# Kernel tuning notes

Hardware: AMD Instinct MI355X
Metric: run time of the kernel (lower is better)

The kernel has to match this reference:

```python
import jax, jax.numpy as jnp
import numpy as np

D = 1024        # d_model
H = 4           # num_heads
DK = D          # key_dim   (expand_k = 1.0)
DV = 2 * D      # value_dim (expand_v = 2.0)
HK = DK // H    # per-head key dim
HV = DV // H    # per-head value dim
KCONV = 4       # short conv kernel size
EPS = 1e-5
CHUNK = 64      # scan chunk size (checkpointing granularity)


def causal_conv_silu(x, w):
    # x: [B,T,C], w: [C,K] depthwise causal conv followed by silu
    B, T, C = x.shape
    K = w.shape[1]
    xp = jnp.pad(x, ((0, 0), (K - 1, 0), (0, 0)))
    y = sum(xp[:, i:i + T, :] * w[:, i] for i in range(K))
    return jax.nn.silu(y)


def l2norm(x):
    return x * jax.lax.rsqrt(jnp.sum(x * x, -1, keepdims=True) + 1e-6)


def _step(S, inp):
    # gated delta rule, one time step. S: [B,H,HK,HV]
    q_t, k_t, v_t, g_t, b_t = inp  # [B,H,HK],[B,H,HK],[B,H,HV],[B,H],[B,H]
    S = S * jnp.exp(g_t)[..., None, None]
    v_eff = (v_t - jnp.einsum('bhk,bhkv->bhv', k_t, S)) * b_t[..., None]
    S = S + k_t[..., None] * v_eff[..., None, :]
    o_t = jnp.einsum('bhk,bhkv->bhv', q_t, S)
    return S, o_t


@jax.checkpoint
def _chunk(S, ch):
    return jax.lax.scan(_step, S, ch)


def _forward(x, ln_w, ln_b, Wq, Wk, Wv, conv_q, conv_k, conv_v, Wb, Wa,
             A_log, dt_bias, Wg, norm_w, Wo):
    B, T, _ = x.shape
    # pre-LayerNorm
    mu = jnp.mean(x, -1, keepdims=True)
    var = jnp.mean((x - mu) ** 2, -1, keepdims=True)
    normed = (x - mu) * jax.lax.rsqrt(var + EPS) * ln_w + ln_b
    # projections + short conv + silu
    q = causal_conv_silu(normed @ Wq, conv_q)
    k = causal_conv_silu(normed @ Wk, conv_k)
    v = causal_conv_silu(normed @ Wv, conv_v)
    beta = jax.nn.sigmoid(normed @ Wb)                                # [B,T,H]
    g = -jnp.exp(A_log) * jax.nn.softplus(normed @ Wa + dt_bias)      # [B,T,H]
    q = l2norm(q.reshape(B, T, H, HK)) * (HK ** -0.5)
    k = l2norm(k.reshape(B, T, H, HK))
    v = v.reshape(B, T, H, HV)
    # chunked sequential scan over time
    nc = T // CHUNK
    def to_chunks(a):
        return jnp.moveaxis(a, 1, 0).reshape((nc, CHUNK, B) + a.shape[2:])
    qc, kc, vc, gc, bc = map(to_chunks, (q, k, v, g, beta))
    S0 = jnp.zeros((B, H, HK, HV), x.dtype)
    _, o = jax.lax.scan(_chunk, S0, (qc, kc, vc, gc, bc))
    o = jnp.moveaxis(o.reshape(T, B, H, HV), 0, 1)                    # [B,T,H,HV]
    # RMSNorm-swish output gate
    g_out = (normed @ Wg).reshape(B, T, H, HV)
    o = o * jax.lax.rsqrt(jnp.mean(o * o, -1, keepdims=True) + EPS) * norm_w
    o = o * g_out * jax.nn.sigmoid(g_out)
    return x + o.reshape(B, T, DV) @ Wo


def setup_inputs() -> dict:
    key = jax.random.key(0)
    ks = jax.random.split(key, 16)
    B, T = 4, 2048
    p = lambda k, shape, s=0.02: jax.random.normal(k, shape, jnp.float32) * s
    return {
        'x': jax.random.normal(ks[0], (B, T, D), jnp.float32),
        'ln_w': jnp.ones((D,), jnp.float32),
        'ln_b': jnp.zeros((D,), jnp.float32),
        'Wq': p(ks[1], (D, DK)),
        'Wk': p(ks[2], (D, DK)),
        'Wv': p(ks[3], (D, DV)),
        'conv_q': p(ks[4], (DK, KCONV), 0.1),
        'conv_k': p(ks[5], (DK, KCONV), 0.1),
        'conv_v': p(ks[6], (DV, KCONV), 0.1),
        'Wb': p(ks[7], (D, H)),
        'Wa': p(ks[8], (D, H)),
        'A_log': jnp.log(jax.random.uniform(ks[9], (H,), jnp.float32, 1.0, 16.0)),
        'dt_bias': jnp.log(jnp.expm1(jax.random.uniform(ks[10], (H,), jnp.float32, 0.001, 0.1))),
        'Wg': p(ks[11], (D, DV)),
        'norm_w': jnp.ones((HV,), jnp.float32),
        'Wo': p(ks[12], (DV, D)),
    }


def reference(x, ln_w, ln_b, Wq, Wk, Wv, conv_q, conv_k, conv_v, Wb, Wa,
              A_log, dt_bias, Wg, norm_w, Wo):
    return _forward(x, ln_w, ln_b, Wq, Wk, Wv, conv_q, conv_k, conv_v,
                    Wb, Wa, A_log, dt_bias, Wg, norm_w, Wo)
```

## Files before the change

### kernel.cpp

```cpp
#include <hip/hip_runtime.h>
#include <math.h>

#define BB 4
#define TT 2048
#define RTOT 8192
#define DD 1024
#define HH 4
#define DKC 1024
#define DVC 2048
#define HKC 256
#define HVC 512
#define NC 32
#define TILE_CV 32

typedef unsigned short u16;
typedef unsigned int u32;
typedef short bf8v __attribute__((ext_vector_type(8)));
typedef float f32x4 __attribute__((ext_vector_type(4)));

__device__ __forceinline__ float bf2f(u16 u) {
    union { float f; u32 i; } c; c.i = ((u32)u) << 16; return c.f;
}
__device__ __forceinline__ u16 f2bf(float f) {
    union { float f; u32 i; } c; c.f = f;
    const u32 i = c.i;
    return (u16)((i + 0x7FFFu + ((i >> 16) & 1u)) >> 16);
}
__device__ __forceinline__ float sigmoidf_(float x) { return 1.0f / (1.0f + expf(-x)); }
__device__ __forceinline__ f32x4 mfma16(bf8v a, bf8v b, f32x4 c) {
    return __builtin_amdgcn_mfma_f32_16x16x32_bf16(a, b, c, 0, 0, 0);
}

__global__ __launch_bounds__(256) void ln_kernel(const float* __restrict__ x,
                                                 const float* __restrict__ w,
                                                 const float* __restrict__ b,
                                                 u16* __restrict__ out) {
    const int row = blockIdx.x;
    const int tid = threadIdx.x;
    const int lane = tid & 63, wave = tid >> 6;
    const float4 xv = *(const float4*)&x[(size_t)row * DD + tid * 4];
    float s = xv.x + xv.y + xv.z + xv.w;
    float sq = xv.x * xv.x + xv.y * xv.y + xv.z * xv.z + xv.w * xv.w;
    for (int m = 32; m >= 1; m >>= 1) {
        s += __shfl_xor(s, m, 64);
        sq += __shfl_xor(sq, m, 64);
    }
    __shared__ float s1[4], s2[4];
    if (lane == 0) { s1[wave] = s; s2[wave] = sq; }
    __syncthreads();
    const float tot = s1[0] + s1[1] + s1[2] + s1[3];
    const float totq = s2[0] + s2[1] + s2[2] + s2[3];
    const float mean = tot * (1.0f / DD);
    const float var = totq * (1.0f / DD) - mean * mean;
    const float rstd = rsqrtf(var + 1e-5f);
    const float4 wv = *(const float4*)&w[tid * 4];
    const float4 bv = *(const float4*)&b[tid * 4];
    ushort4 o;
    o.x = f2bf((xv.x - mean) * rstd * wv.x + bv.x);
    o.y = f2bf((xv.y - mean) * rstd * wv.y + bv.y);
    o.z = f2bf((xv.z - mean) * rstd * wv.z + bv.z);
    o.w = f2bf((xv.w - mean) * rstd * wv.w + bv.w);
    *(ushort4*)&out[(size_t)row * DD + tid * 4] = o;
}

__global__ __launch_bounds__(256) void wconv_kernel(const float* __restrict__ W,
                                                    u16* __restrict__ WT, int K, int N) {
    __shared__ float tile[32][33];
    const int k0 = blockIdx.x * 32, n0 = blockIdx.y * 32;
    const int t = threadIdx.x;
    const int r = t >> 3, c4 = (t & 7) * 4;
    const float4 v = *(const float4*)&W[(size_t)(k0 + r) * N + n0 + c4];
    tile[r][c4 + 0] = v.x; tile[r][c4 + 1] = v.y;
    tile[r][c4 + 2] = v.z; tile[r][c4 + 3] = v.w;
    __syncthreads();
    ushort4 o;
    o.x = f2bf(tile[c4 + 0][r]); o.y = f2bf(tile[c4 + 1][r]);
    o.z = f2bf(tile[c4 + 2][r]); o.w = f2bf(tile[c4 + 3][r]);
    *(ushort4*)&WT[(size_t)(n0 + r) * K + k0 + c4] = o;
}

template <int OUTMODE>
__global__ __launch_bounds__(256, 2) void gemm_mfma(const u16* __restrict__ A,
                                                    const u16* __restrict__ BT,
                                                    void* __restrict__ Cv,
                                                    int M, int N, int K,
                                                    const float* __restrict__ Res) {
    __shared__ u16 As[128][40];
    __shared__ u16 Bs[128][40];
    const int tid = threadIdx.x;
    const int wave = tid >> 6, lane = tid & 63;
    const int quad = lane >> 4, l15 = lane & 15;
    const int wr = wave >> 1, wc = wave & 1;
    const int bn = blockIdx.x, bm = blockIdx.y;
    const int srow = tid >> 1, sh = (tid & 1) * 16;
    const u16* Ap = A + (size_t)(bm * 128 + srow) * K + sh;
    const u16* Bp = BT + (size_t)(bn * 128 + srow) * K + sh;
    f32x4 acc[4][4];
#pragma unroll
    for (int i = 0; i < 4; ++i)
#pragma unroll
        for (int j = 0; j < 4; ++j) acc[i][j] = (f32x4){0.f, 0.f, 0.f, 0.f};

    for (int k0 = 0; k0 < K; k0 += 32) {
        const bf8v a0 = *(const bf8v*)(Ap + k0);
        const bf8v a1 = *(const bf8v*)(Ap + k0 + 8);
        const bf8v b0 = *(const bf8v*)(Bp + k0);
        const bf8v b1 = *(const bf8v*)(Bp + k0 + 8);
        __syncthreads();
        *(bf8v*)&As[srow][sh] = a0;
        *(bf8v*)&As[srow][sh + 8] = a1;
        *(bf8v*)&Bs[srow][sh] = b0;
        *(bf8v*)&Bs[srow][sh + 8] = b1;
        __syncthreads();
        bf8v af[4], bfr[4];
#pragma unroll
        for (int i = 0; i < 4; ++i) af[i] = *(const bf8v*)&As[wr * 64 + i * 16 + l15][quad * 8];
#pragma unroll
        for (int j = 0; j < 4; ++j) bfr[j] = *(const bf8v*)&Bs[wc * 64 + j * 16 + l15][quad * 8];
#pragma unroll
        for (int i = 0; i < 4; ++i)
#pragma unroll
            for (int j = 0; j < 4; ++j)
                acc[i][j] = mfma16(af[i], bfr[j], acc[i][j]);
    }
#pragma unroll
    for (int i = 0; i < 4; ++i) {
        const int row = bm * 128 + wr * 64 + i * 16 + quad * 4;
#pragma unroll
        for (int j = 0; j < 4; ++j) {
            const int col = bn * 128 + wc * 64 + j * 16 + l15;
            if (OUTMODE == 0) {
                u16* C = (u16*)Cv;
#pragma unroll
                for (int r = 0; r < 4; ++r)
                    C[(size_t)(row + r) * N + col] = f2bf(acc[i][j][r]);
            } else {
                float* C = (float*)Cv;
#pragma unroll
                for (int r = 0; r < 4; ++r)
                    C[(size_t)(row + r) * N + col] = acc[i][j][r] + Res[(size_t)(row + r) * N + col];
            }
        }
    }
}

__global__ __launch_bounds__(256) void smallproj_kernel(const float* __restrict__ x,
                                                        const float* __restrict__ lnw,
                                                        const float* __restrict__ lnb,
                                                        const float* __restrict__ Wb,
                                                        const float* __restrict__ Wa,
                                                        const float* __restrict__ A_log,
                                                        const float* __restrict__ dt_bias,
                                                        float* __restrict__ beta,
                                                        float* __restrict__ gdec) {
    const int row = blockIdx.x;
    const int tid = threadIdx.x;
    const int lane = tid & 63, wave = tid >> 6;
    const float4 xv = *(const float4*)&x[(size_t)row * DD + tid * 4];
    float s = xv.x + xv.y + xv.z + xv.w;
    float sq = xv.x * xv.x + xv.y * xv.y + xv.z * xv.z + xv.w * xv.w;
    for (int m = 32; m >= 1; m >>= 1) {
        s += __shfl_xor(s, m, 64);
        sq += __shfl_xor(sq, m, 64);
    }
    __shared__ float s1[4], s2[4];
    if (lane == 0) { s1[wave] = s; s2[wave] = sq; }
    __syncthreads();
    const float mean = (s1[0] + s1[1] + s1[2] + s1[3]) * (1.0f / DD);
    const float var = (s2[0] + s2[1] + s2[2] + s2[3]) * (1.0f / DD) - mean * mean;
    const float rstd = rsqrtf(var + 1e-5f);
    const float4 wv = *(const float4*)&lnw[tid * 4];
    const float4 bv = *(const float4*)&lnb[tid * 4];
    float nv[4];
    nv[0] = (xv.x - mean) * rstd * wv.x + bv.x;
    nv[1] = (xv.y - mean) * rstd * wv.y + bv.y;
    nv[2] = (xv.z - mean) * rstd * wv.z + bv.z;
    nv[3] = (xv.w - mean) * rstd * wv.w + bv.w;
    float acc[8] = {};
#pragma unroll
    for (int j = 0; j < 4; ++j) {
        const int kk = tid * 4 + j;
        const float4 wb = ((const float4*)Wb)[kk];
        const float4 wa = ((const float4*)Wa)[kk];
        acc[0] += nv[j] * wb.x; acc[1] += nv[j] * wb.y; acc[2] += nv[j] * wb.z; acc[3] += nv[j] * wb.w;
        acc[4] += nv[j] * wa.x; acc[5] += nv[j] * wa.y; acc[6] += nv[j] * wa.z; acc[7] += nv[j] * wa.w;
    }
#pragma unroll
    for (int i = 0; i < 8; ++i)
        for (int m = 32; m >= 1; m >>= 1) acc[i] += __shfl_xor(acc[i], m, 64);
    __shared__ float sred[4][8];
    if (lane == 0)
#pragma unroll
        for (int i = 0; i < 8; ++i) sred[wave][i] = acc[i];
    __syncthreads();
    if (tid < 8) {
        const float sv = sred[0][tid] + sred[1][tid] + sred[2][tid] + sred[3][tid];
        if (tid < 4) {
            beta[(size_t)row * HH + tid] = 1.0f / (1.0f + expf(-sv));
        } else {
            const int h = tid - 4;
            const float z = sv + dt_bias[h];
            const float sp = (z > 20.0f) ? z : log1pf(expf(z));
            gdec[(size_t)row * HH + h] = -expf(A_log[h]) * sp;
        }
    }
}

__global__ __launch_bounds__(256) void halo_save(const u16* __restrict__ P,
                                                 u16* __restrict__ halo, int C) {
    const int tt = blockIdx.x;
    const int r0 = tt * TILE_CV;
    const int t0 = r0 & (TT - 1);
    const int n4 = (3 * C) >> 2;
    for (int idx = threadIdx.x; idx < n4; idx += 256) {
        const int flat = idx * 4;
        const int j = flat / C;
        const int c = flat - j * C;
        ushort4 vv;
        if (t0 == 0) { vv.x = vv.y = vv.z = vv.w = 0; }
        else vv = *(const ushort4*)&P[(size_t)(r0 - 1 - j) * C + c];
        *(ushort4*)&halo[(size_t)(tt * 3 + j) * C + c] = vv;
    }
}

__global__ __launch_bounds__(256) void conv_inplace(u16* __restrict__ P,
                                                    const float* __restrict__ w,
                                                    const u16* __restrict__ halo, int C) {
    const int tt = blockIdx.y;
    const int r0 = tt * TILE_CV;
    const int c0 = blockIdx.x * 1024 + threadIdx.x * 4;
    float wt[4][4];
#pragma unroll
    for (int j = 0; j < 4; ++j)
#pragma unroll
        for (int i = 0; i < 4; ++i) wt[j][i] = w[(c0 + j) * 4 + i];
    float xm1[4], xm2[4], xm3[4];
    {
        const ushort4 h0 = *(const ushort4*)&halo[(size_t)(tt * 3 + 0) * C + c0];
        const ushort4 h1 = *(const ushort4*)&halo[(size_t)(tt * 3 + 1) * C + c0];
        const ushort4 h2 = *(const ushort4*)&halo[(size_t)(tt * 3 + 2) * C + c0];
        xm1[0] = bf2f(h0.x); xm1[1] = bf2f(h0.y); xm1[2] = bf2f(h0.z); xm1[3] = bf2f(h0.w);
        xm2[0] = bf2f(h1.x); xm2[1] = bf2f(h1.y); xm2[2] = bf2f(h1.z); xm2[3] = bf2f(h1.w);
        xm3[0] = bf2f(h2.x); xm3[1] = bf2f(h2.y); xm3[2] = bf2f(h2.z); xm3[3] = bf2f(h2.w);
    }
    for (int t = 0; t < TILE_CV; ++t) {
        u16* rowp = P + (size_t)(r0 + t) * C + c0;
        const ushort4 cv = *(const ushort4*)rowp;
        float cur[4] = {bf2f(cv.x), bf2f(cv.y), bf2f(cv.z), bf2f(cv.w)};
        ushort4 ov;
        u16* op = (u16*)&ov;
#pragma unroll
        for (int j = 0; j < 4; ++j) {
            const float y = xm3[j] * wt[j][0] + xm2[j] * wt[j][1] + xm1[j] * wt[j][2] + cur[j] * wt[j][3];
            op[j] = f2bf(y * sigmoidf_(y));
        }
        *(ushort4*)rowp = ov;
#pragma unroll
        for (int j = 0; j < 4; ++j) { xm3[j] = xm2[j]; xm2[j] = xm1[j]; xm1[j] = cur[j]; }
    }
}

__global__ __launch_bounds__(256) void normqk_kernel(u16* __restrict__ q, u16* __restrict__ k) {
    const int row = blockIdx.x;
    const int tid = threadIdx.x;
    const int h = tid >> 6, lane = tid & 63;
    const size_t base = (size_t)row * DKC + h * HKC + lane * 4;
    const ushort4 q4 = *(ushort4*)&q[base];
    const ushort4 k4 = *(ushort4*)&k[base];
    float qv[4] = {bf2f(q4.x), bf2f(q4.y), bf2f(q4.z), bf2f(q4.w)};
    float kv[4] = {bf2f(k4.x), bf2f(k4.y), bf2f(k4.z), bf2f(k4.w)};
    float sq = qv[0]*qv[0] + qv[1]*qv[1] + qv[2]*qv[2] + qv[3]*qv[3];
    float sk = kv[0]*kv[0] + kv[1]*kv[1] + kv[2]*kv[2] + kv[3]*kv[3];
    for (int m = 32; m >= 1; m >>= 1) {
        sq += __shfl_xor(sq, m, 64);
        sk += __shfl_xor(sk, m, 64);
    }
    const float qs = rsqrtf(sq + 1e-6f) * 0.0625f;
    const float ks = rsqrtf(sk + 1e-6f);
    ushort4 qo, ko;
    qo.x = f2bf(qv[0]*qs); qo.y = f2bf(qv[1]*qs); qo.z = f2bf(qv[2]*qs); qo.w = f2bf(qv[3]*qs);
    ko.x = f2bf(kv[0]*ks); ko.y = f2bf(kv[1]*ks); ko.z = f2bf(kv[2]*ks); ko.w = f2bf(kv[3]*ks);
    *(ushort4*)&q[base] = qo;
    *(ushort4*)&k[base] = ko;
}

__global__ __launch_bounds__(256) void p1a_kernel(const u16* __restrict__ qg,
                                                  const u16* __restrict__ kg,
                                                  const float* __restrict__ gdec,
                                                  const float* __restrict__ beta,
                                                  u16* __restrict__ Mg,
                                                  u16* __restrict__ Pg,
                                                  u16* __restrict__ kTg,
                                                  float* __restrict__ gcg) {
    __shared__ float T[64][68];
    __shared__ float Mm[64][68];
    __shared__ float gcs[64], bars[64];
    const int CI = blockIdx.x;
    const int c = CI & 31, h = (CI >> 5) & 3, b = CI >> 7;
    const int tid = threadIdx.x, lane = tid & 63, wave = tid >> 6;
    const int quad = lane >> 4, l15 = lane & 15;
    const int rowbase = b * TT + c * 64;
    if (wave == 0) {
        float g = gdec[(size_t)(rowbase + lane) * HH + h];
        for (int d = 1; d < 64; d <<= 1) { float o2 = __shfl_up(g, d, 64); if (lane >= d) g += o2; }
        gcs[lane] = g;
        bars[lane] = beta[(size_t)(rowbase + lane) * HH + h];
        gcg[CI * 64 + lane] = g;
    }
    __syncthreads();
    const int t0 = wave * 16;
    bf8v I0, I16;
#pragma unroll
    for (int j = 0; j < 8; ++j) {
        ((u16*)&I0)[j]  = (quad * 8 + j == l15)      ? (u16)0x3F80 : (u16)0;
        ((u16*)&I16)[j] = (quad * 8 + j == l15 + 16) ? (u16)0x3F80 : (u16)0;
    }
    f32x4 kk[4], qk[4];
#pragma unroll
    for (int st = 0; st < 4; ++st) { kk[st] = (f32x4){0,0,0,0}; qk[st] = (f32x4){0,0,0,0}; }
    const size_t arow = (size_t)(rowbase + t0 + l15) * DKC + h * HKC + quad * 8;
    for (int ks = 0; ks < 8; ++ks) {
        const bf8v ak = *(const bf8v*)(kg + arow + ks * 32);
        const bf8v aq = *(const bf8v*)(qg + arow + ks * 32);
        f32x4 tr0 = (f32x4){0,0,0,0}, tr1 = (f32x4){0,0,0,0};
        tr0 = mfma16(I0, ak, tr0);
        tr1 = mfma16(I16, ak, tr1);
        const size_t kbase = (size_t)CI * 16384 + t0 + l15;
#pragma unroll
        for (int i = 0; i < 4; ++i) {
            kTg[kbase + (size_t)(ks * 32 + quad * 4 + i) * 64] = f2bf(tr0[i]);
            kTg[kbase + (size_t)(ks * 32 + 16 + quad * 4 + i) * 64] = f2bf(tr1[i]);
        }
#pragma unroll
        for (int st = 0; st < 4; ++st) {
            const size_t brow = (size_t)(rowbase + st * 16 + l15) * DKC + h * HKC + quad * 8 + ks * 32;
            const bf8v bk = *(const bf8v*)(kg + brow);
            kk[st] = mfma16(ak, bk, kk[st]);
            qk[st] = mfma16(aq, bk, qk[st]);
        }
    }
#pragma unroll
    for (int st = 0; st < 4; ++st)
#pragma unroll
        for (int i = 0; i < 4; ++i) {
            const int t = t0 + quad * 4 + i, s = st * 16 + l15;
            const float e = expf(gcs[t] - gcs[s]);
            T[t][s] = (s < t) ? bars[t] * e * kk[st][i] : 0.f;
            Pg[(size_t)CI * 4096 + t * 64 + s] = f2bf((s <= t) ? e * qk[st][i] : 0.f);
        }
    __syncthreads();
    if (wave == 0) {
        const int j = lane;
        Mm[0][j] = (j == 0) ? 1.f : 0.f;
        for (int t = 1; t < 64; ++t) {
            float acc = 0.f;
            for (int s = 0; s < t; ++s) acc += T[t][s] * Mm[s][j];
            Mm[t][j] = ((t == j) ? 1.f : 0.f) - acc;
        }
    }
    __syncthreads();
    for (int idx = tid; idx < 4096; idx += 256)
        Mg[(size_t)CI * 4096 + idx] = f2bf(Mm[idx >> 6][idx & 63]);
}

__global__ __launch_bounds__(512) void p2_kernel(const u16* __restrict__ qg,
                                                 const u16* __restrict__ kg,
                                                 const u16* __restrict__ vg,
                                                 const float* __restrict__ beta,
                                                 const float* __restrict__ gcg,
                                                 const u16* __restrict__ Mg,
                                                 const u16* __restrict__ Pg,
                                                 const u16* __restrict__ kTg,
                                                 u16* __restrict__ og) {
    __shared__ u16 SbT[2][32][264];
    __shared__ u16 uT[32][72];
    __shared__ u16 vT[32][72];
    __shared__ u16 v2T[32][72];
    const int bid = blockIdx.x;
    const int vs = bid & 15, h = (bid >> 4) & 3, b = bid >> 6;
    const int tid = threadIdx.x, lane = tid & 63, wave = tid >> 6;
    const int quad = lane >> 4, l15 = lane & 15;
    const int tw = wave >> 1, nw = wave & 1;
    const int t0 = tw * 16;
    const int ncol = nw * 16 + l15;
    for (int i = tid; i < 32 * 264; i += 512) ((u16*)SbT[0])[i] = 0;
    f32x4 S[4];
#pragma unroll
    for (int a = 0; a < 4; ++a) S[a] = (f32x4){0,0,0,0};
    __syncthreads();

    for (int c = 0; c < NC; ++c) {
        const int cur = c & 1, nxt = cur ^ 1;
        const int CI = (b * 4 + h) * NC + c;
        const int rowbase = b * TT + c * 64;
        const float gc63 = gcg[CI * 64 + 63];
        float bt[4], ga[4], gd[4];
#pragma unroll
        for (int i = 0; i < 4; ++i) {
            const int t = t0 + quad * 4 + i;
            bt[i] = beta[(size_t)(rowbase + t) * HH + h];
            const float gc = gcg[CI * 64 + t];
            ga[i] = expf(gc);
            gd[i] = expf(gc63 - gc);
        }
        const size_t krow = (size_t)(rowbase + t0 + l15) * DKC + h * HKC + quad * 8;
        f32x4 ka0 = (f32x4){0,0,0,0}, ka1 = (f32x4){0,0,0,0};
        for (int ks = 0; ks < 8; ks += 2) {
            const bf8v ak0 = *(const bf8v*)(kg + krow + ks * 32);
            const bf8v ak1 = *(const bf8v*)(kg + krow + ks * 32 + 32);
            const bf8v bs0 = *(const bf8v*)(&SbT[cur][ncol][ks * 32 + quad * 8]);
            const bf8v bs1 = *(const bf8v*)(&SbT[cur][ncol][ks * 32 + 32 + quad * 8]);
            ka0 = mfma16(ak0, bs0, ka0);
            ka1 = mfma16(ak1, bs1, ka1);
        }
        {
            ushort4 up; u16* upp = (u16*)&up;
#pragma unroll
            for (int i = 0; i < 4; ++i) {
                const int t = t0 + quad * 4 + i;
                const float vv = bf2f(vg[(size_t)(rowbase + t) * DVC + h * HVC + vs * 32 + ncol]);
                upp[i] = f2bf(bt[i] * vv - bt[i] * ga[i] * (ka0[i] + ka1[i]));
            }
            *(ushort4*)(&uT[ncol][t0 + quad * 4]) = up;
        }
        __syncthreads();
        f32x4 vacc = (f32x4){0,0,0,0};
        for (int ks = 0; ks < 2; ++ks) {
            const bf8v am = *(const bf8v*)(Mg + (size_t)CI * 4096 + (t0 + l15) * 64 + ks * 32 + quad * 8);
            const bf8v bu = *(const bf8v*)(&uT[ncol][ks * 32 + quad * 8]);
            vacc = mfma16(am, bu, vacc);
        }
        {
            ushort4 vp, v2p; u16* vpp = (u16*)&vp; u16* v2pp = (u16*)&v2p;
#pragma unroll
            for (int i = 0; i < 4; ++i) {
                vpp[i] = f2bf(vacc[i]);
                v2pp[i] = f2bf(vacc[i] * gd[i]);
            }
            *(ushort4*)(&vT[ncol][t0 + quad * 4]) = vp;
            *(ushort4*)(&v2T[ncol][t0 + quad * 4]) = v2p;
        }
        __syncthreads();
        f32x4 op_ = (f32x4){0,0,0,0};
        for (int ks = 0; ks < 2; ++ks) {
            const bf8v ap = *(const bf8v*)(Pg + (size_t)CI * 4096 + (t0 + l15) * 64 + ks * 32 + quad * 8);
            const bf8v bv_ = *(const bf8v*)(&vT[ncol][ks * 32 + quad * 8]);
            op_ = mfma16(ap, bv_, op_);
        }
        f32x4 oq0 = (f32x4){0,0,0,0}, oq1 = (f32x4){0,0,0,0};
        const size_t qrow = (size_t)(rowbase + t0 + l15) * DKC + h * HKC + quad * 8;
        for (int ks = 0; ks < 8; ks += 2) {
            const bf8v aq0 = *(const bf8v*)(qg + qrow + ks * 32);
            const bf8v aq1 = *(const bf8v*)(qg + qrow + ks * 32 + 32);
            const bf8v bs0 = *(const bf8v*)(&SbT[cur][ncol][ks * 32 + quad * 8]);
            const bf8v bs1 = *(const bf8v*)(&SbT[cur][ncol][ks * 32 + 32 + quad * 8]);
            oq0 = mfma16(aq0, bs0, oq0);
            oq1 = mfma16(aq1, bs1, oq1);
        }
#pragma unroll
        for (int i = 0; i < 4; ++i) {
            const int t = t0 + quad * 4 + i;
            og[((size_t)(b * 4 + h) * TT + c * 64 + t) * HVC + vs * 32 + ncol] =
                f2bf(op_[i] + ga[i] * (oq0[i] + oq1[i]));
        }
        const float gC = expf(gc63);
#pragma unroll
        for (int a = 0; a < 4; ++a) {
            const int r0 = (tw * 4 + a) * 16;
            f32x4 acc = S[a] * gC;
            for (int ks = 0; ks < 2; ++ks) {
                const bf8v akt = *(const bf8v*)(kTg + (size_t)CI * 16384 + (r0 + l15) * 64 + ks * 32 + quad * 8);
                const bf8v bv2 = *(const bf8v*)(&v2T[ncol][ks * 32 + quad * 8]);
                acc = mfma16(akt, bv2, acc);
            }
            S[a] = acc;
            ushort4 sp; u16* spp = (u16*)&sp;
#pragma unroll
            for (int i = 0; i < 4; ++i) spp[i] = f2bf(acc[i]);
            *(ushort4*)(&SbT[nxt][ncol][r0 + quad * 4]) = sp;
        }
        __syncthreads();
    }
}

__global__ __launch_bounds__(256) void gate_kernel(const u16* __restrict__ o,
                                                   u16* __restrict__ pg,
                                                   const float* __restrict__ norm_w) {
    const int row = blockIdx.x;
    const int b = row >> 11, t = row & 2047;
    const int tid = threadIdx.x;
    const int h = tid >> 6, lane = tid & 63;
    const size_t obase = ((size_t)(b * 4 + h) * TT + t) * HVC + lane * 4;
    const size_t pbase = (size_t)row * DVC + h * HVC + lane * 4;
    const ushort4 a4 = *(const ushort4*)&o[obase];
    const ushort4 b4 = *(const ushort4*)&o[obase + 256];
    float o1[4] = {bf2f(a4.x), bf2f(a4.y), bf2f(a4.z), bf2f(a4.w)};
    float o2[4] = {bf2f(b4.x), bf2f(b4.y), bf2f(b4.z), bf2f(b4.w)};
    float ss = 0.f;
#pragma unroll
    for (int j = 0; j < 4; ++j) ss += o1[j]*o1[j] + o2[j]*o2[j];
    for (int m = 32; m >= 1; m >>= 1) ss += __shfl_xor(ss, m, 64);
    const float rms = rsqrtf(ss * (1.0f / HVC) + 1e-5f);
    const float4 nw1 = *(const float4*)&norm_w[lane * 4];
    const float4 nw2 = *(const float4*)&norm_w[256 + lane * 4];
    const ushort4 g4a = *(const ushort4*)&pg[pbase];
    const ushort4 g4b = *(const ushort4*)&pg[pbase + 256];
    const float g1[4] = {bf2f(g4a.x), bf2f(g4a.y), bf2f(g4a.z), bf2f(g4a.w)};
    const float g2[4] = {bf2f(g4b.x), bf2f(g4b.y), bf2f(g4b.z), bf2f(g4b.w)};
    const float n1[4] = {nw1.x, nw1.y, nw1.z, nw1.w};
    const float n2[4] = {nw2.x, nw2.y, nw2.z, nw2.w};
    ushort4 r1, r2;
    u16* p1 = (u16*)&r1; u16* p2 = (u16*)&r2;
#pragma unroll
    for (int j = 0; j < 4; ++j) {
        p1[j] = f2bf(o1[j] * rms * n1[j] * g1[j] * sigmoidf_(g1[j]));
        p2[j] = f2bf(o2[j] * rms * n2[j] * g2[j] * sigmoidf_(g2[j]));
    }
    *(ushort4*)&pg[pbase] = r1;
    *(ushort4*)&pg[pbase + 256] = r2;
}

extern "C" void kernel_launch(void* const* d_in, const int* in_sizes, int n_in,
                              void* d_out, int out_size, void* d_ws, size_t ws_size,
                              hipStream_t stream) {
    const float* x       = (const float*)d_in[0];
    const float* ln_w    = (const float*)d_in[1];
    const float* ln_b    = (const float*)d_in[2];
    const float* Wq      = (const float*)d_in[3];
    const float* Wk      = (const float*)d_in[4];
    const float* Wv      = (const float*)d_in[5];
    const float* conv_q  = (const float*)d_in[6];
    const float* conv_k  = (const float*)d_in[7];
    const float* conv_v  = (const float*)d_in[8];
    const float* Wb      = (const float*)d_in[9];
    const float* Wa      = (const float*)d_in[10];
    const float* A_log   = (const float*)d_in[11];
    const float* dt_bias = (const float*)d_in[12];
    const float* Wg      = (const float*)d_in[13];
    const float* norm_w  = (const float*)d_in[14];
    const float* Wo      = (const float*)d_in[15];
    float* out = (float*)d_out;

    char* ws = (char*)d_ws;
    u16* normed = (u16*)(ws);
    u16* q      = (u16*)(ws + (16ull << 20));
    u16* k      = (u16*)(ws + (32ull << 20));
    u16* v      = (u16*)(ws + (48ull << 20));
    u16* o      = (u16*)(ws + (80ull << 20));
    float* beta = (float*)(ws + (112ull << 20));
    float* gdec = (float*)(ws + (112ull << 20) + (128u<<10));
    float* gcg  = (float*)(ws + (112ull << 20) + (256u<<10));
    u16* halo   = (u16*)(ws + (113ull << 20));
    u16* Mg     = (u16*)(ws + (116ull << 20));
    u16* Pg     = (u16*)(ws + (120ull << 20));
    u16* pg     = q;
    u16* WTe    = o;
    u16* WgT    = Mg;
    u16* WoT    = v;
    u16* kTg    = (u16*)d_out;

    ln_kernel<<<RTOT, 256, 0, stream>>>(x, ln_w, ln_b, normed);

    wconv_kernel<<<dim3(DD / 32, DKC / 32), 256, 0, stream>>>(Wq, WTe, DD, DKC);
    gemm_mfma<0><<<dim3(DKC / 128, RTOT / 128), 256, 0, stream>>>(normed, WTe, q, RTOT, DKC, DD, nullptr);
    wconv_kernel<<<dim3(DD / 32, DKC / 32), 256, 0, stream>>>(Wk, WTe, DD, DKC);
    gemm_mfma<0><<<dim3(DKC / 128, RTOT / 128), 256, 0, stream>>>(normed, WTe, k, RTOT, DKC, DD, nullptr);
    wconv_kernel<<<dim3(DD / 32, DVC / 32), 256, 0, stream>>>(Wv, WTe, DD, DVC);
    gemm_mfma<0><<<dim3(DVC / 128, RTOT / 128), 256, 0, stream>>>(normed, WTe, v, RTOT, DVC, DD, nullptr);
    smallproj_kernel<<<RTOT, 256, 0, stream>>>(x, ln_w, ln_b, Wb, Wa, A_log, dt_bias, beta, gdec);

    halo_save<<<RTOT / TILE_CV, 256, 0, stream>>>(q, halo, DKC);
    conv_inplace<<<dim3(1, RTOT / TILE_CV), 256, 0, stream>>>(q, conv_q, halo, DKC);
    halo_save<<<RTOT / TILE_CV, 256, 0, stream>>>(k, halo, DKC);
    conv_inplace<<<dim3(1, RTOT / TILE_CV), 256, 0, stream>>>(k, conv_k, halo, DKC);
    halo_save<<<RTOT / TILE_CV, 256, 0, stream>>>(v, halo, DVC);
    conv_inplace<<<dim3(2, RTOT / TILE_CV), 256, 0, stream>>>(v, conv_v, halo, DVC);

    normqk_kernel<<<RTOT, 256, 0, stream>>>(q, k);

    p1a_kernel<<<BB * HH * NC, 256, 0, stream>>>(q, k, gdec, beta, Mg, Pg, kTg, gcg);
    p2_kernel<<<BB * HH * (HVC / 32), 512, 0, stream>>>(q, k, v, beta, gcg, Mg, Pg, kTg, o);

    wconv_kernel<<<dim3(DD / 32, DVC / 32), 256, 0, stream>>>(Wg, WgT, DD, DVC);
    gemm_mfma<0><<<dim3(DVC / 128, RTOT / 128), 256, 0, stream>>>(normed, WgT, pg, RTOT, DVC, DD, nullptr);

    gate_kernel<<<RTOT, 256, 0, stream>>>(o, pg, norm_w);

    wconv_kernel<<<dim3(DVC / 32, DD / 32), 256, 0, stream>>>(Wo, WoT, DVC, DD);
    gemm_mfma<1><<<dim3(DD / 128, RTOT / 128), 256, 0, stream>>>(pg, WoT, out, RTOT, DD, DVC, x);
}
```

Before: 793.1 us.

## Prefetch per-chunk operands into registers and remap blocks for cache sharing

The sequential chunk-scan kernel now issues all global loads for a chunk (M, P, q, kT fragments) at the top of the iteration, and prefetches the next chunk's k and v during the current one. This takes global-memory latency off the serial dependency chain between barriers. The block index is also remapped so that the 16 value-slice blocks sharing a (b,h) pair are spread across the grid, which changes how L2 is shared. The added register arrays increase VGPR pressure and could reduce occupancy or cause spills.

```diff
diff --git a/kernel.cpp b/kernel.cpp
--- a/kernel.cpp
+++ b/kernel.cpp
@@ -377,7 +377,8 @@
     __shared__ u16 vT[32][72];
     __shared__ u16 v2T[32][72];
     const int bid = blockIdx.x;
-    const int vs = bid & 15, h = (bid >> 4) & 3, b = bid >> 6;
+    const int bh = bid & 15, vs = bid >> 4;
+    const int h = bh & 3, b = bh >> 2;
     const int tid = threadIdx.x, lane = tid & 63, wave = tid >> 6;
     const int quad = lane >> 4, l15 = lane & 15;
     const int tw = wave >> 1, nw = wave & 1;
@@ -387,12 +388,38 @@
     f32x4 S[4];
 #pragma unroll
     for (int a = 0; a < 4; ++a) S[a] = (f32x4){0,0,0,0};
+
+    bf8v kf[8]; u16 vf[4];
+    {
+        const int rowbase = b * TT;
+        const size_t krow = (size_t)(rowbase + t0 + l15) * DKC + h * HKC + quad * 8;
+#pragma unroll
+        for (int ks = 0; ks < 8; ++ks) kf[ks] = *(const bf8v*)(kg + krow + ks * 32);
+#pragma unroll
+        for (int i = 0; i < 4; ++i)
+            vf[i] = vg[(size_t)(rowbase + t0 + quad * 4 + i) * DVC + h * HVC + vs * 32 + ncol];
+    }
     __syncthreads();
 
     for (int c = 0; c < NC; ++c) {
         const int cur = c & 1, nxt = cur ^ 1;
-        const int CI = (b * 4 + h) * NC + c;
+        const int CI = bh * NC + c;
         const int rowbase = b * TT + c * 64;
+        bf8v Mf[2], Pf[2], qf[8], kTf[8];
+#pragma unroll
+        for (int ks = 0; ks < 2; ++ks) {
+            Mf[ks] = *(const bf8v*)(Mg + (size_t)CI * 4096 + (t0 + l15) * 64 + ks * 32 + quad * 8);
+            Pf[ks] = *(const bf8v*)(Pg + (size_t)CI * 4096 + (t0 + l15) * 64 + ks * 32 + quad * 8);
+        }
+        const size_t qrow = (size_t)(rowbase + t0 + l15) * DKC + h * HKC + quad * 8;
+#pragma unroll
+        for (int ks = 0; ks < 8; ++ks) qf[ks] = *(const bf8v*)(qg + qrow + ks * 32);
+#pragma unroll
+        for (int a = 0; a < 4; ++a)
+#pragma unroll
+            for (int ks = 0; ks < 2; ++ks)
+                kTf[a * 2 + ks] = *(const bf8v*)(kTg + (size_t)CI * 16384 +
+                                                 (size_t)((tw * 4 + a) * 16 + l15) * 64 + ks * 32 + quad * 8);
         const float gc63 = gcg[CI * 64 + 63];
         float bt[4], ga[4], gd[4];
 #pragma unroll
@@ -403,32 +430,34 @@
             ga[i] = expf(gc);
             gd[i] = expf(gc63 - gc);
         }
-        const size_t krow = (size_t)(rowbase + t0 + l15) * DKC + h * HKC + quad * 8;
         f32x4 ka0 = (f32x4){0,0,0,0}, ka1 = (f32x4){0,0,0,0};
         for (int ks = 0; ks < 8; ks += 2) {
-            const bf8v ak0 = *(const bf8v*)(kg + krow + ks * 32);
-            const bf8v ak1 = *(const bf8v*)(kg + krow + ks * 32 + 32);
             const bf8v bs0 = *(const bf8v*)(&SbT[cur][ncol][ks * 32 + quad * 8]);
             const bf8v bs1 = *(const bf8v*)(&SbT[cur][ncol][ks * 32 + 32 + quad * 8]);
-            ka0 = mfma16(ak0, bs0, ka0);
-            ka1 = mfma16(ak1, bs1, ka1);
+            ka0 = mfma16(kf[ks], bs0, ka0);
+            ka1 = mfma16(kf[ks + 1], bs1, ka1);
         }
         {
             ushort4 up; u16* upp = (u16*)&up;
 #pragma unroll
-            for (int i = 0; i < 4; ++i) {
-                const int t = t0 + quad * 4 + i;
-                const float vv = bf2f(vg[(size_t)(rowbase + t) * DVC + h * HVC + vs * 32 + ncol]);
-                upp[i] = f2bf(bt[i] * vv - bt[i] * ga[i] * (ka0[i] + ka1[i]));
-            }
+            for (int i = 0; i < 4; ++i)
+                upp[i] = f2bf(bt[i] * bf2f(vf[i]) - bt[i] * ga[i] * (ka0[i] + ka1[i]));
             *(ushort4*)(&uT[ncol][t0 + quad * 4]) = up;
+        }
+        if (c + 1 < NC) {
+            const int rb2 = b * TT + (c + 1) * 64;
+            const size_t krow2 = (size_t)(rb2 + t0 + l15) * DKC + h * HKC + quad * 8;
+#pragma unroll
+            for (int ks = 0; ks < 8; ++ks) kf[ks] = *(const bf8v*)(kg + krow2 + ks * 32);
+#pragma unroll
+            for (int i = 0; i < 4; ++i)
+                vf[i] = vg[(size_t)(rb2 + t0 + quad * 4 + i) * DVC + h * HVC + vs * 32 + ncol];
         }
         __syncthreads();
         f32x4 vacc = (f32x4){0,0,0,0};
         for (int ks = 0; ks < 2; ++ks) {
-            const bf8v am = *(const bf8v*)(Mg + (size_t)CI * 4096 + (t0 + l15) * 64 + ks * 32 + quad * 8);
             const bf8v bu = *(const bf8v*)(&uT[ncol][ks * 32 + quad * 8]);
-            vacc = mfma16(am, bu, vacc);
+            vacc = mfma16(Mf[ks], bu, vacc);
         }
         {
             ushort4 vp, v2p; u16* vpp = (u16*)&vp; u16* v2pp = (u16*)&v2p;
@@ -443,24 +472,20 @@
         __syncthreads();
         f32x4 op_ = (f32x4){0,0,0,0};
         for (int ks = 0; ks < 2; ++ks) {
-            const bf8v ap = *(const bf8v*)(Pg + (size_t)CI * 4096 + (t0 + l15) * 64 + ks * 32 + quad * 8);
             const bf8v bv_ = *(const bf8v*)(&vT[ncol][ks * 32 + quad * 8]);
-            op_ = mfma16(ap, bv_, op_);
+            op_ = mfma16(Pf[ks], bv_, op_);
         }
         f32x4 oq0 = (f32x4){0,0,0,0}, oq1 = (f32x4){0,0,0,0};
-        const size_t qrow = (size_t)(rowbase + t0 + l15) * DKC + h * HKC + quad * 8;
         for (int ks = 0; ks < 8; ks += 2) {
-            const bf8v aq0 = *(const bf8v*)(qg + qrow + ks * 32);
-            const bf8v aq1 = *(const bf8v*)(qg + qrow + ks * 32 + 32);
             const bf8v bs0 = *(const bf8v*)(&SbT[cur][ncol][ks * 32 + quad * 8]);
             const bf8v bs1 = *(const bf8v*)(&SbT[cur][ncol][ks * 32 + 32 + quad * 8]);
-            oq0 = mfma16(aq0, bs0, oq0);
-            oq1 = mfma16(aq1, bs1, oq1);
+            oq0 = mfma16(qf[ks], bs0, oq0);
+            oq1 = mfma16(qf[ks + 1], bs1, oq1);
         }
 #pragma unroll
         for (int i = 0; i < 4; ++i) {
             const int t = t0 + quad * 4 + i;
-            og[((size_t)(b * 4 + h) * TT + c * 64 + t) * HVC + vs * 32 + ncol] =
+            og[((size_t)bh * TT + c * 64 + t) * HVC + vs * 32 + ncol] =
                 f2bf(op_[i] + ga[i] * (oq0[i] + oq1[i]));
         }
         const float gC = expf(gc63);
@@ -469,9 +494,8 @@
             const int r0 = (tw * 4 + a) * 16;
             f32x4 acc = S[a] * gC;
             for (int ks = 0; ks < 2; ++ks) {
-                const bf8v akt = *(const bf8v*)(kTg + (size_t)CI * 16384 + (r0 + l15) * 64 + ks * 32 + quad * 8);
                 const bf8v bv2 = *(const bf8v*)(&v2T[ncol][ks * 32 + quad * 8]);
-                acc = mfma16(akt, bv2, acc);
+                acc = mfma16(kTf[a * 2 + ks], bv2, acc);
             }
             S[a] = acc;
             ushort4 sp; u16* spp = (u16*)&sp;
```

Result: faster. 756.8 us (-4.6%).
